# Performance work log

Hardware: AMD Instinct MI355X
Metric: run time of the kernel (lower is better)

## Reference

```python
import jax, jax.numpy as jnp
import numpy as np

N = 50000
E = 800000
D_IN = 384
D_H = 128
D_MLP = 128
K = 16


def layer_norm(x, g, b, eps=1e-5):
    m = x.mean(-1, keepdims=True)
    v = ((x - m) ** 2).mean(-1, keepdims=True)
    return (x - m) / jnp.sqrt(v + eps) * g + b


def setup_inputs() -> dict:
    key = jax.random.key(0)
    ks = jax.random.split(key, 16)
    s = lambda d: 1.0 / np.sqrt(d)
    return {
        "x": jax.random.normal(ks[0], (N, D_IN), jnp.float32),
        "edge_index": jax.random.randint(ks[1], (2, E), 0, N, jnp.int64),
        # GCNConv 1
        "W1": jax.random.normal(ks[2], (D_IN, D_H), jnp.float32) * s(D_IN),
        "b1": jnp.zeros((D_H,), jnp.float32),
        "g1": jnp.ones((D_H,), jnp.float32),
        "be1": jnp.zeros((D_H,), jnp.float32),
        # GCNConv 2
        "W2": jax.random.normal(ks[3], (D_H, D_H), jnp.float32) * s(D_H),
        "b2": jnp.zeros((D_H,), jnp.float32),
        "g2": jnp.ones((D_H,), jnp.float32),
        "be2": jnp.zeros((D_H,), jnp.float32),
        # residual projection (input_dim != conv_hidden)
        "rW": jax.random.normal(ks[4], (D_IN, D_H), jnp.float32) * s(D_IN),
        "rb": jnp.zeros((D_H,), jnp.float32),
        "rg": jnp.ones((D_H,), jnp.float32),
        "rbe": jnp.zeros((D_H,), jnp.float32),
        # MLP head
        "mW1": jax.random.normal(ks[5], (D_H, D_MLP), jnp.float32) * s(D_H),
        "mb1": jnp.zeros((D_MLP,), jnp.float32),
        "mg": jnp.ones((D_MLP,), jnp.float32),
        "mbe": jnp.zeros((D_MLP,), jnp.float32),
        "mW2": jax.random.normal(ks[6], (D_MLP, K), jnp.float32) * s(D_MLP),
        "mb2": jnp.zeros((K,), jnp.float32),
    }


def reference(x, edge_index, W1, b1, g1, be1, W2, b2, g2, be2,
              rW, rb, rg, rbe, mW1, mb1, mg, mbe, mW2, mb2):
    n = x.shape[0]
    loops = jnp.arange(n, dtype=edge_index.dtype)
    src = jnp.concatenate([edge_index[0], loops])  # [E+N]
    dst = jnp.concatenate([edge_index[1], loops])
    # symmetric GCN normalization with self-loops
    deg = jax.ops.segment_sum(jnp.ones_like(src, x.dtype), dst, num_segments=n)
    dinv = jnp.where(deg > 0, jax.lax.rsqrt(deg), 0.0)
    norm = dinv[src] * dinv[dst]  # [E+N]

    def gcn_conv(h, W, b):
        hw = h @ W  # [N, D_H]
        msg = hw[src] * norm[:, None]  # gather + scale, [E+N, D_H]
        return jax.ops.segment_sum(msg, dst, num_segments=n) + b

    # layer 1 with projected residual
    h = jax.nn.elu(layer_norm(gcn_conv(x, W1, b1), g1, be1))
    h = h + layer_norm(x @ rW + rb, rg, rbe)
    # layer 2 with identity residual
    h = jax.nn.elu(layer_norm(gcn_conv(h, W2, b2), g2, be2)) + h
    # MLP head (dropout inactive in eval) + softmax over clusters
    z = jax.nn.elu(layer_norm(h @ mW1 + mb1, mg, mbe))
    H = z @ mW2 + mb2
    return jax.nn.softmax(H, axis=1)
```

## Files before the change

kernel.cpp:

```cpp
#include <hip/hip_runtime.h>

#define DH 128

typedef __attribute__((ext_vector_type(8))) short short8;
typedef __attribute__((ext_vector_type(4))) float f32x4;

__device__ __forceinline__ float wave_sum(float v) {
    #pragma unroll
    for (int o = 32; o > 0; o >>= 1) v += __shfl_xor(v, o, 64);
    return v;
}

__device__ __forceinline__ void ln_pair(float v0, float v1, float& o0, float& o1) {
    float m = wave_sum(v0 + v1) * (1.f / 128.f);
    float d0 = v0 - m, d1 = v1 - m;
    float var = wave_sum(d0 * d0 + d1 * d1) * (1.f / 128.f);
    float inv = rsqrtf(var + 1e-5f);
    o0 = d0 * inv; o1 = d1 * inv;
}

__device__ __forceinline__ float elu(float x) { return x > 0.f ? x : expm1f(x); }

__device__ __forceinline__ unsigned short f2bf(float f) {
    unsigned u = __float_as_uint(f);
    u += 0x7fffu + ((u >> 16) & 1u);
    return (unsigned short)(u >> 16);
}
__device__ __forceinline__ float bfl(unsigned u) { return __uint_as_float(u << 16); }
__device__ __forceinline__ float bfh(unsigned u) { return __uint_as_float(u & 0xffff0000u); }
__device__ __forceinline__ unsigned pack_bf2(float a, float b) {
    return (unsigned)f2bf(a) | ((unsigned)f2bf(b) << 16);
}
__device__ __forceinline__ short8 cvt8(float4 v0, float4 v1) {
    short8 o;
    o[0] = (short)f2bf(v0.x); o[1] = (short)f2bf(v0.y);
    o[2] = (short)f2bf(v0.z); o[3] = (short)f2bf(v0.w);
    o[4] = (short)f2bf(v1.x); o[5] = (short)f2bf(v1.y);
    o[6] = (short)f2bf(v1.z); o[7] = (short)f2bf(v1.w);
    return o;
}

__device__ __forceinline__ int xcd_work(int bid, int nwg) {
    int qc = nwg >> 3, rc = nwg & 7;
    int xcd = bid & 7, ix = bid >> 3;
    return (xcd < rc ? xcd * (qc + 1) : rc * (qc + 1) + (xcd - rc) * qc) + ix;
}

__device__ __forceinline__ void gload_lds16(const void* gp, void* lp) {
    __builtin_amdgcn_global_load_lds(
        (const __attribute__((address_space(1))) void*)gp,
        (__attribute__((address_space(3))) void*)lp, 16, 0, 0);
}

__global__ void deg_count_k(const int* __restrict__ dst, int* __restrict__ deg, int E) {
    int e = blockIdx.x * 256 + threadIdx.x;
    if (e < E) atomicAdd(&deg[dst[e]], 1);
}

__global__ __launch_bounds__(1024) void scan_part_k(const int* __restrict__ deg,
                                                    int* __restrict__ rowptr,
                                                    int* __restrict__ bsum,
                                                    float* __restrict__ dinv, int n)
{
    __shared__ int wsum[16];
    const int tid = threadIdx.x, lane = tid & 63, wid = tid >> 6;
    int i = blockIdx.x * 1024 + tid;
    int v = (i < n) ? deg[i] : 0;
    if (i < n) dinv[i] = rsqrtf((float)(v + 1));
    int s = v;
    #pragma unroll
    for (int o = 1; o < 64; o <<= 1) {
        int t = __shfl_up(s, o, 64);
        if (lane >= o) s += t;
    }
    if (lane == 63) wsum[wid] = s;
    __syncthreads();
    if (tid < 16) {
        int ws = wsum[tid];
        #pragma unroll
        for (int o = 1; o < 16; o <<= 1) {
            int t = __shfl_up(ws, o, 64);
            if (tid >= o) ws += t;
        }
        wsum[tid] = ws;
    }
    __syncthreads();
    int excl = (wid ? wsum[wid - 1] : 0) + s - v;
    if (i < n) rowptr[i] = excl;
    if (tid == 0) bsum[blockIdx.x] = wsum[15];
}

__global__ void scan_top_k(int* __restrict__ bsum, int* __restrict__ rowptr_n, int nb) {
    int lane = threadIdx.x;
    int carry = 0;
    for (int base = 0; base < nb; base += 64) {
        int i = base + lane;
        int v = (i < nb) ? bsum[i] : 0;
        int s = v;
        #pragma unroll
        for (int o = 1; o < 64; o <<= 1) {
            int t = __shfl_up(s, o, 64);
            if (lane >= o) s += t;
        }
        if (i < nb) bsum[i] = carry + s - v;
        carry += __shfl(s, 63, 64);
    }
    if (lane == 0) *rowptr_n = carry;
}

__global__ void scan_add_k(const int* __restrict__ bsum, int* __restrict__ rowptr,
                           int* __restrict__ cursor, int n)
{
    int i = blockIdx.x * 256 + threadIdx.x;
    if (i < n) {
        int v = rowptr[i] + bsum[i >> 10];
        rowptr[i] = v;
        cursor[i] = v;
    }
}

__global__ __launch_bounds__(256) void fill_xcd_k(
    const int* __restrict__ src, const int* __restrict__ dst,
    const float* __restrict__ dinv, int* __restrict__ cursor,
    int2* __restrict__ csr, int E, int n)
{
    const int g   = blockIdx.x & 7;
    const int j   = blockIdx.x >> 3;
    const int bpg = gridDim.x >> 3;
    const int per = (n + 7) >> 3;
    const int lo = g * per;
    const int hi = min(n, lo + per);
    for (int e = j * 256 + threadIdx.x; e < E; e += bpg * 256) {
        int d = dst[e];
        if (d >= lo && d < hi) {
            int s = src[e];
            float w = dinv[s] * dinv[d];
            int p = atomicAdd(&cursor[d], 1);
            csr[p] = make_int2(s, __float_as_int(w));
        }
    }
}

__global__ void repack_zero_k(const float* __restrict__ W1, const float* __restrict__ rW,
                              const float* __restrict__ W2, const float* __restrict__ mW1,
                              unsigned short* __restrict__ Wp, int* __restrict__ deg, int n)
{
    int idx = blockIdx.x * 256 + threadIdx.x;
    if (idx < n) deg[idx] = 0;
    if (idx >= 131072) return;
    const float* W; int base;
    if (idx < 49152)       { W = W1;  base = 0; }
    else if (idx < 98304)  { W = rW;  base = 49152; }
    else if (idx < 114688) { W = W2;  base = 98304; }
    else                   { W = mW1; base = 114688; }
    int l = idx - base;
    int kb = l >> 12, rem = l & 4095;
    int nn = rem >> 5, ki = rem & 31;
    Wp[idx] = f2bf(W[(kb * 32 + ki) * DH + nn]);
}

__global__ __launch_bounds__(256, 2) void gemm1_k(
    const float* __restrict__ x,
    const unsigned short* __restrict__ Bp1, const unsigned short* __restrict__ Bp2,
    const float* __restrict__ bb,
    unsigned short* __restrict__ outa, unsigned short* __restrict__ outb, int n)
{
    constexpr int NT = 6;
    __shared__ __align__(16) unsigned char smraw[81920];
    float* smA = (float*)smraw;
    unsigned short* smB = (unsigned short*)(smraw + 65536);

    const int tid = threadIdx.x;
    const int wid = tid >> 6, lane = tid & 63;
    const int m16 = lane & 15, q = lane >> 4;

    const int work = xcd_work(blockIdx.x, gridDim.x);
    const int rblk = work >> 2;
    const int var  = work & 3;
    const int mat = var >> 1;
    const int c0  = (var & 1) * 64;
    const unsigned short* Bp = mat ? Bp2 : Bp1;
    unsigned short* outp = mat ? outb : outa;
    const float* bias = mat ? bb : nullptr;
    const long long rowbase = (long long)rblk * 128;

    const float* gA[8];
    int ldsA[8];
    #pragma unroll
    for (int i = 0; i < 8; ++i) {
        int j = wid * 8 + i;
        int r = j * 4 + (lane >> 4);
        int c = lane & 15;
        long long gr = rowbase + r; if (gr > (long long)n - 1) gr = n - 1;
        gA[i] = x + gr * 384 + ((c ^ (r & 15)) * 4);
        ldsA[i] = j * 256;
    }
    const unsigned short* gB[2];
    int ldsB[2];
    #pragma unroll
    for (int i = 0; i < 2; ++i) {
        int j2 = wid * 2 + i;
        int cl = j2 * 8 + (lane >> 3);
        int c = lane & 7;
        int cp = c ^ (cl & 7);
        gB[i] = Bp + (cp >> 2) * 4096 + (c0 + cl) * 32 + (cp & 3) * 8;
        ldsB[i] = j2 * 512;
    }

    auto issueT = [&](int t, int buf) {
        #pragma unroll
        for (int i = 0; i < 8; ++i)
            gload_lds16(gA[i] + t * 64, smA + buf * 8192 + ldsA[i]);
        #pragma unroll
        for (int i = 0; i < 2; ++i)
            gload_lds16(gB[i] + t * 8192, smB + buf * 4096 + ldsB[i]);
    };

    f32x4 acc[2][4];
    const f32x4 zero = {0.f, 0.f, 0.f, 0.f};
    #pragma unroll
    for (int mi = 0; mi < 2; ++mi)
        #pragma unroll
        for (int nj = 0; nj < 4; ++nj) acc[mi][nj] = zero;

    const int arow = wid * 32 + m16;
    const int s8b = m16 & 7;

    issueT(0, 0);
    __syncthreads();

    #pragma unroll
    for (int t = 0; t < NT; ++t) {
        const int buf = t & 1;
        if (t + 1 < NT) issueT(t + 1, buf ^ 1);
        const float* a0 = smA + buf * 8192;
        const unsigned short* b0 = smB + buf * 4096;
        short8 af[2][2], bf[2][4];
        #pragma unroll
        for (int ks = 0; ks < 2; ++ks) {
            int g0 = ks * 8 + q * 2;
            {
                float4 lo = *(const float4*)(a0 + arow * 64 + ((g0 ^ m16) * 4));
                float4 hi = *(const float4*)(a0 + arow * 64 + (((g0 + 1) ^ m16) * 4));
                af[ks][0] = cvt8(lo, hi);
            }
            {
                float4 lo = *(const float4*)(a0 + (arow + 16) * 64 + ((g0 ^ m16) * 4));
                float4 hi = *(const float4*)(a0 + (arow + 16) * 64 + (((g0 + 1) ^ m16) * 4));
                af[ks][1] = cvt8(lo, hi);
            }
            int co = ((ks * 4 + q) ^ s8b) * 8;
            #pragma unroll
            for (int nj = 0; nj < 4; ++nj)
                bf[ks][nj] = *(const short8*)(b0 + (nj * 16 + m16) * 64 + co);
        }
        #pragma unroll
        for (int ks = 0; ks < 2; ++ks)
            #pragma unroll
            for (int nj = 0; nj < 4; ++nj) {
                acc[0][nj] = __builtin_amdgcn_mfma_f32_16x16x32_bf16(af[ks][0], bf[ks][nj], acc[0][nj], 0, 0, 0);
                acc[1][nj] = __builtin_amdgcn_mfma_f32_16x16x32_bf16(af[ks][1], bf[ks][nj], acc[1][nj], 0, 0, 0);
            }
        __syncthreads();
    }

    unsigned short* ep = (unsigned short*)smraw;
    #pragma unroll
    for (int nj = 0; nj < 4; ++nj) {
        int cl = nj * 16 + m16;
        float bv = bias ? bias[c0 + cl] : 0.f;
        #pragma unroll
        for (int mi = 0; mi < 2; ++mi)
            #pragma unroll
            for (int r = 0; r < 4; ++r)
                ep[(wid * 32 + mi * 16 + q * 4 + r) * 72 + cl] = f2bf(acc[mi][nj][r] + bv);
    }
    __syncthreads();
    #pragma unroll
    for (int h = 0; h < 4; ++h) {
        int idx = tid + h * 256;
        int row = idx >> 3, c8 = idx & 7;
        long long grow = rowbase + row;
        if (grow < n)
            *(short8*)(outp + grow * DH + c0 + c8 * 8) = *(const short8*)(ep + row * 72 + c8 * 8);
    }
}

__global__ __launch_bounds__(256, 3) void gemm_k128(
    const unsigned short* __restrict__ A,
    const unsigned short* __restrict__ Bp, const float* __restrict__ bias,
    unsigned short* __restrict__ outp, int n)
{
    __shared__ __align__(16) unsigned short smem[24576];
    unsigned short* smB = smem + 16384;

    const int tid = threadIdx.x;
    const int wid = tid >> 6, lane = tid & 63;
    const int m16 = lane & 15, q = lane >> 4;

    const int work = xcd_work(blockIdx.x, gridDim.x);
    const int rblk = work >> 1;
    const int c0 = (work & 1) * 64;
    const long long rowbase = (long long)rblk * 128;

    #pragma unroll
    for (int r = 0; r < 8; ++r) {
        int j = r * 256 + tid;
        int row = j >> 4, c16 = j & 15;
        long long grow = rowbase + row; if (grow > (long long)n - 1) grow = n - 1;
        *(short8*)(smem + row * 128 + ((c16 ^ (row & 15)) * 8)) =
            *(const short8*)(A + grow * 128 + c16 * 8);
    }
    #pragma unroll
    for (int r = 0; r < 4; ++r) {
        int j = r * 256 + tid;
        int kb = j >> 8, rem = j & 255;
        int cl = rem >> 2, qq = rem & 3;
        *(short8*)(smB + kb * 2048 + qq * 512 + cl * 8) =
            *(const short8*)(Bp + kb * 4096 + c0 * 32 + rem * 8);
    }
    __syncthreads();

    f32x4 acc[2][4];
    const f32x4 zero = {0.f, 0.f, 0.f, 0.f};
    #pragma unroll
    for (int mi = 0; mi < 2; ++mi)
        #pragma unroll
        for (int nj = 0; nj < 4; ++nj) acc[mi][nj] = zero;

    const int frow = wid * 32 + m16;
    #pragma unroll
    for (int kb = 0; kb < 4; ++kb) {
        short8 af0 = *(const short8*)(smem + frow * 128 + (((kb * 4 + q) ^ m16) * 8));
        short8 af1 = *(const short8*)(smem + (frow + 16) * 128 + (((kb * 4 + q) ^ m16) * 8));
        #pragma unroll
        for (int nj = 0; nj < 4; ++nj) {
            short8 bf = *(const short8*)(smB + kb * 2048 + q * 512 + (nj * 16 + m16) * 8);
            acc[0][nj] = __builtin_amdgcn_mfma_f32_16x16x32_bf16(af0, bf, acc[0][nj], 0, 0, 0);
            acc[1][nj] = __builtin_amdgcn_mfma_f32_16x16x32_bf16(af1, bf, acc[1][nj], 0, 0, 0);
        }
    }

    __syncthreads();
    #pragma unroll
    for (int nj = 0; nj < 4; ++nj) {
        int cl = nj * 16 + m16;
        float bv = bias ? bias[c0 + cl] : 0.f;
        #pragma unroll
        for (int mi = 0; mi < 2; ++mi)
            #pragma unroll
            for (int r = 0; r < 4; ++r)
                smem[(wid * 32 + mi * 16 + q * 4 + r) * 72 + cl] = f2bf(acc[mi][nj][r] + bv);
    }
    __syncthreads();
    #pragma unroll
    for (int h = 0; h < 4; ++h) {
        int idx = tid + h * 256;
        int row = idx >> 3, c8 = idx & 7;
        long long grow = rowbase + row;
        if (grow < n)
            *(short8*)(outp + grow * DH + c0 + c8 * 8) = *(const short8*)(smem + row * 72 + c8 * 8);
    }
}

__device__ __forceinline__ void gather_row(
    const unsigned* __restrict__ hw, const int2* __restrict__ csr,
    int beg, int end, int lane, float& o0, float& o1)
{
    beg = __builtin_amdgcn_readfirstlane(beg);
    end = __builtin_amdgcn_readfirstlane(end);
    float a0 = 0.f, a1 = 0.f, b0 = 0.f, b1 = 0.f;
    float c0 = 0.f, c1 = 0.f, d0 = 0.f, d1 = 0.f;
    int p = beg;
    for (; p + 15 < end; p += 16) {
        int2 e[16];
        #pragma unroll
        for (int i = 0; i < 16; ++i) e[i] = csr[p + i];
        unsigned u[16];
        #pragma unroll
        for (int i = 0; i < 16; ++i) u[i] = hw[(long long)e[i].x * 64 + lane];
        #pragma unroll
        for (int i = 0; i < 16; ++i) {
            float w = __int_as_float(e[i].y);
            float lo = bfl(u[i]), hi = bfh(u[i]);
            if ((i & 3) == 0)      { a0 = fmaf(w, lo, a0); a1 = fmaf(w, hi, a1); }
            else if ((i & 3) == 1) { b0 = fmaf(w, lo, b0); b1 = fmaf(w, hi, b1); }
            else if ((i & 3) == 2) { c0 = fmaf(w, lo, c0); c1 = fmaf(w, hi, c1); }
            else                   { d0 = fmaf(w, lo, d0); d1 = fmaf(w, hi, d1); }
        }
    }
    for (; p + 3 < end; p += 4) {
        int2 e0 = csr[p], e1 = csr[p + 1], e2 = csr[p + 2], e3 = csr[p + 3];
        unsigned u0 = hw[(long long)e0.x * 64 + lane];
        unsigned u1 = hw[(long long)e1.x * 64 + lane];
        unsigned u2 = hw[(long long)e2.x * 64 + lane];
        unsigned u3 = hw[(long long)e3.x * 64 + lane];
        float w0 = __int_as_float(e0.y), w1 = __int_as_float(e1.y);
        float w2 = __int_as_float(e2.y), w3 = __int_as_float(e3.y);
        a0 = fmaf(w0, bfl(u0), a0);  a1 = fmaf(w0, bfh(u0), a1);
        b0 = fmaf(w1, bfl(u1), b0);  b1 = fmaf(w1, bfh(u1), b1);
        c0 = fmaf(w2, bfl(u2), c0);  c1 = fmaf(w2, bfh(u2), c1);
        d0 = fmaf(w3, bfl(u3), d0);  d1 = fmaf(w3, bfh(u3), d1);
    }
    for (; p < end; ++p) {
        int2 e0 = csr[p];
        unsigned u0 = hw[(long long)e0.x * 64 + lane];
        float w0 = __int_as_float(e0.y);
        a0 = fmaf(w0, bfl(u0), a0);
        a1 = fmaf(w0, bfh(u0), a1);
    }
    o0 = (a0 + b0) + (c0 + d0);
    o1 = (a1 + b1) + (c1 + d1);
}

__global__ __launch_bounds__(256) void gfuse1_k(
    const unsigned* __restrict__ hw, const unsigned* __restrict__ proj,
    const int* __restrict__ rowptr, const int2* __restrict__ csr,
    const float* __restrict__ dinv,
    const float* __restrict__ b1, const float* __restrict__ g1, const float* __restrict__ be1,
    const float* __restrict__ rg, const float* __restrict__ rbe,
    unsigned* __restrict__ hout, int n)
{
    int row = blockIdx.x * 4 + (threadIdx.x >> 6);
    if (row >= n) return;
    int lane = threadIdx.x & 63;
    float a0, a1;
    gather_row(hw, csr, rowptr[row], rowptr[row + 1], lane, a0, a1);
    long long off = (long long)row * 64;
    float di = dinv[row], sl = di * di;
    unsigned us = hw[off + lane];
    float2 bv  = *(const float2*)(b1 + 2 * lane);
    float2 gv  = *(const float2*)(g1 + 2 * lane);
    float2 bev = *(const float2*)(be1 + 2 * lane);
    float2 rgv = *(const float2*)(rg + 2 * lane);
    float2 rbv = *(const float2*)(rbe + 2 * lane);
    float v0 = a0 + sl * bfl(us) + bv.x;
    float v1 = a1 + sl * bfh(us) + bv.y;
    float o0, o1; ln_pair(v0, v1, o0, o1);
    float t0 = elu(o0 * gv.x + bev.x);
    float t1 = elu(o1 * gv.y + bev.y);
    unsigned up = proj[off + lane];
    float q0, q1; ln_pair(bfl(up), bfh(up), q0, q1);
    hout[off + lane] = pack_bf2(t0 + q0 * rgv.x + rbv.x, t1 + q1 * rgv.y + rbv.y);
}

__global__ __launch_bounds__(256) void gfuse2_k(
    const unsigned* __restrict__ hw, const unsigned* __restrict__ hprev,
    const int* __restrict__ rowptr, const int2* __restrict__ csr,
    const float* __restrict__ dinv,
    const float* __restrict__ b2, const float* __restrict__ g2, const float* __restrict__ be2,
    unsigned* __restrict__ h2, int n)
{
    int row = blockIdx.x * 4 + (threadIdx.x >> 6);
    if (row >= n) return;
    int lane = threadIdx.x & 63;
    float a0, a1;
    gather_row(hw, csr, rowptr[row], rowptr[row + 1], lane, a0, a1);
    long long off = (long long)row * 64;
    float di = dinv[row], sl = di * di;
    unsigned us = hw[off + lane];
    float2 bv  = *(const float2*)(b2 + 2 * lane);
    float2 gv  = *(const float2*)(g2 + 2 * lane);
    float2 bev = *(const float2*)(be2 + 2 * lane);
    float v0 = a0 + sl * bfl(us) + bv.x;
    float v1 = a1 + sl * bfh(us) + bv.y;
    float o0, o1; ln_pair(v0, v1, o0, o1);
    float t0 = elu(o0 * gv.x + bev.x);
    float t1 = elu(o1 * gv.y + bev.y);
    unsigned uh = hprev[off + lane];
    h2[off + lane] = pack_bf2(t0 + bfl(uh), t1 + bfh(uh));
}

__global__ __launch_bounds__(256) void head_k(
    const unsigned* __restrict__ zraw, const float* __restrict__ g, const float* __restrict__ be,
    const float* __restrict__ mW2, const float* __restrict__ mb2,
    float* __restrict__ out, int n)
{
    int row = blockIdx.x * 4 + (threadIdx.x >> 6);
    if (row >= n) return;
    int lane = threadIdx.x & 63;
    unsigned u = zraw[(long long)row * 64 + lane];
    float o0, o1; ln_pair(bfl(u), bfh(u), o0, o1);
    float2 gv  = *(const float2*)(g + 2 * lane);
    float2 bev = *(const float2*)(be + 2 * lane);
    float z0 = elu(o0 * gv.x + bev.x);
    float z1 = elu(o1 * gv.y + bev.y);
    int k = lane & 15, seg = lane >> 4;
    float acc = 0.f;
    #pragma unroll
    for (int t = 0; t < 16; ++t) {
        int srcl = seg * 16 + t;
        float zz0 = __shfl(z0, srcl, 64);
        float zz1 = __shfl(z1, srcl, 64);
        int c = seg * 32 + 2 * t;
        acc = fmaf(zz0, mW2[c * 16 + k], acc);
        acc = fmaf(zz1, mW2[(c + 1) * 16 + k], acc);
    }
    acc += __shfl_xor(acc, 32, 64);
    acc += __shfl_xor(acc, 16, 64);
    float hk = acc + mb2[k];
    float mx = hk;
    #pragma unroll
    for (int o = 8; o > 0; o >>= 1) mx = fmaxf(mx, __shfl_xor(mx, o, 64));
    float e = expf(hk - mx);
    float s = e;
    #pragma unroll
    for (int o = 8; o > 0; o >>= 1) s += __shfl_xor(s, o, 64);
    if (lane < 16) out[(long long)row * 16 + k] = e / s;
}

static inline size_t align16(size_t x) { return (x + 15) & ~(size_t)15; }

extern "C" void kernel_launch(void* const* d_in, const int* in_sizes, int n_in,
                              void* d_out, int out_size, void* d_ws, size_t ws_size,
                              hipStream_t stream)
{
    const float* x   = (const float*)d_in[0];
    const int*   ei  = (const int*)d_in[1];
    const float* W1  = (const float*)d_in[2];
    const float* b1  = (const float*)d_in[3];
    const float* g1  = (const float*)d_in[4];
    const float* be1 = (const float*)d_in[5];
    const float* W2  = (const float*)d_in[6];
    const float* b2  = (const float*)d_in[7];
    const float* g2  = (const float*)d_in[8];
    const float* be2 = (const float*)d_in[9];
    const float* rW  = (const float*)d_in[10];
    const float* rb  = (const float*)d_in[11];
    const float* rg  = (const float*)d_in[12];
    const float* rbe = (const float*)d_in[13];
    const float* mW1 = (const float*)d_in[14];
    const float* mb1 = (const float*)d_in[15];
    const float* mg  = (const float*)d_in[16];
    const float* mbe = (const float*)d_in[17];
    const float* mW2 = (const float*)d_in[18];
    const float* mb2 = (const float*)d_in[19];
    float* out = (float*)d_out;

    const int n = in_sizes[0] / 384;
    const int E = in_sizes[1] / 2;
    const int* src = ei;
    const int* dst = ei + E;

    char* w = (char*)d_ws;
    int* deg     = (int*)w;   w += align16((size_t)n * 4);
    int* rowptr  = (int*)w;   w += align16((size_t)(n + 1) * 4);
    int* cursor  = (int*)w;   w += align16((size_t)n * 4);
    float* dinv  = (float*)w; w += align16((size_t)n * 4);
    int* bsum    = (int*)w;   w += align16((size_t)1024 * 4);
    int2* csr    = (int2*)w;  w += align16((size_t)E * 8);
    unsigned short* hw1  = (unsigned short*)w; w += align16((size_t)n * DH * 2);
    unsigned short* proj = (unsigned short*)w; w += align16((size_t)n * DH * 2);
    unsigned short* hbuf = (unsigned short*)w; w += align16((size_t)n * DH * 2);
    unsigned short* Wp   = (unsigned short*)w; w += align16((size_t)131072 * 2);
    unsigned short* Wp1 = Wp;
    unsigned short* Wpr = Wp + 49152;
    unsigned short* Wp2 = Wp + 98304;
    unsigned short* WpM = Wp + 114688;
    unsigned short* hw2  = hw1;
    unsigned short* h2   = proj;
    unsigned short* zraw = hbuf;

    int gE = (E + 255) / 256;
    int gN = (n + 255) / 256;
    int nb = (n + 1023) / 1024;
    int rblks = (n + 127) / 128;
    int gRow4 = (n + 3) / 4;

    repack_zero_k<<<512, 256, 0, stream>>>(W1, rW, W2, mW1, Wp, deg, n);

    deg_count_k<<<gE, 256, 0, stream>>>(dst, deg, E);
    scan_part_k<<<nb, 1024, 0, stream>>>(deg, rowptr, bsum, dinv, n);
    scan_top_k<<<1, 64, 0, stream>>>(bsum, rowptr + n, nb);
    scan_add_k<<<gN, 256, 0, stream>>>(bsum, rowptr, cursor, n);
    fill_xcd_k<<<1024, 256, 0, stream>>>(src, dst, dinv, cursor, csr, E, n);

    gemm1_k<<<rblks * 4, 256, 0, stream>>>(x, Wp1, Wpr, rb, hw1, proj, n);
    gfuse1_k<<<gRow4, 256, 0, stream>>>((unsigned*)hw1, (unsigned*)proj, rowptr, csr, dinv,
                                        b1, g1, be1, rg, rbe, (unsigned*)hbuf, n);

    gemm_k128<<<rblks * 2, 256, 0, stream>>>(hbuf, Wp2, nullptr, hw2, n);
    gfuse2_k<<<gRow4, 256, 0, stream>>>((unsigned*)hw2, (unsigned*)hbuf, rowptr, csr, dinv,
                                        b2, g2, be2, (unsigned*)h2, n);

    gemm_k128<<<rblks * 2, 256, 0, stream>>>(h2, WpM, mb1, zraw, n);
    head_k<<<gRow4, 256, 0, stream>>>((unsigned*)zraw, mg, mbe, mW2, mb2, out, n);
}
```

Measured before the change: 408.1 us.

## Triple-buffer gemm1 with smaller K tiles and partition degree atomics by XCD

The first GEMM now uses 32-wide K tiles (12 steps) in a three-stage LDS ring with explicit vmcnt waits and raw barriers. Prefetch runs two tiles ahead, and the next load is issued after the fragment reads, so global loads overlap the MFMAs and one barrier per step is dropped. LDS use drops from 80KB to 60KB. The degree-count kernel becomes a grid-stride loop in which each XCD group counts only destinations in its own node range, keeping atomics local to one L2. In exchange, every group reads the whole dst array.

```diff
diff --git a/kernel.cpp b/kernel.cpp
--- a/kernel.cpp
+++ b/kernel.cpp
@@ -52,9 +52,19 @@
         (__attribute__((address_space(3))) void*)lp, 16, 0, 0);
 }
 
-__global__ void deg_count_k(const int* __restrict__ dst, int* __restrict__ deg, int E) {
-    int e = blockIdx.x * 256 + threadIdx.x;
-    if (e < E) atomicAdd(&deg[dst[e]], 1);
+__global__ __launch_bounds__(256) void deg_xcd_k(
+    const int* __restrict__ dst, int* __restrict__ deg, int E, int n)
+{
+    const int g   = blockIdx.x & 7;
+    const int j   = blockIdx.x >> 3;
+    const int bpg = gridDim.x >> 3;
+    const int per = (n + 7) >> 3;
+    const int lo = g * per;
+    const int hi = min(n, lo + per);
+    for (int e = j * 256 + threadIdx.x; e < E; e += bpg * 256) {
+        int d = dst[e];
+        if (d >= lo && d < hi) atomicAdd(&deg[d], 1);
+    }
 }
 
 __global__ __launch_bounds__(1024) void scan_part_k(const int* __restrict__ deg,
@@ -165,10 +175,8 @@
     const float* __restrict__ bb,
     unsigned short* __restrict__ outa, unsigned short* __restrict__ outb, int n)
 {
-    constexpr int NT = 6;
-    __shared__ __align__(16) unsigned char smraw[81920];
-    float* smA = (float*)smraw;
-    unsigned short* smB = (unsigned short*)(smraw + 65536);
+    constexpr int NT = 12;
+    __shared__ __align__(16) unsigned char smraw[61440];
 
     const int tid = threadIdx.x;
     const int wid = tid >> 6, lane = tid & 63;
@@ -177,43 +185,34 @@
     const int work = xcd_work(blockIdx.x, gridDim.x);
     const int rblk = work >> 2;
     const int var  = work & 3;
-    const int mat = var >> 1;
-    const int c0  = (var & 1) * 64;
+    const int mat  = var >> 1;
+    const int c0   = (var & 1) * 64;
     const unsigned short* Bp = mat ? Bp2 : Bp1;
     unsigned short* outp = mat ? outb : outa;
     const float* bias = mat ? bb : nullptr;
     const long long rowbase = (long long)rblk * 128;
 
-    const float* gA[8];
-    int ldsA[8];
-    #pragma unroll
-    for (int i = 0; i < 8; ++i) {
-        int j = wid * 8 + i;
-        int r = j * 4 + (lane >> 4);
-        int c = lane & 15;
+    const float* gA[4];
+    int abase[4];
+    #pragma unroll
+    for (int i = 0; i < 4; ++i) {
+        int j = wid * 4 + i;
+        int r = j * 8 + (lane >> 3);
+        int c = lane & 7;
         long long gr = rowbase + r; if (gr > (long long)n - 1) gr = n - 1;
-        gA[i] = x + gr * 384 + ((c ^ (r & 15)) * 4);
-        ldsA[i] = j * 256;
-    }
-    const unsigned short* gB[2];
-    int ldsB[2];
-    #pragma unroll
-    for (int i = 0; i < 2; ++i) {
-        int j2 = wid * 2 + i;
-        int cl = j2 * 8 + (lane >> 3);
-        int c = lane & 7;
-        int cp = c ^ (cl & 7);
-        gB[i] = Bp + (cp >> 2) * 4096 + (c0 + cl) * 32 + (cp & 3) * 8;
-        ldsB[i] = j2 * 512;
-    }
-
-    auto issueT = [&](int t, int buf) {
-        #pragma unroll
-        for (int i = 0; i < 8; ++i)
-            gload_lds16(gA[i] + t * 64, smA + buf * 8192 + ldsA[i]);
-        #pragma unroll
-        for (int i = 0; i < 2; ++i)
-            gload_lds16(gB[i] + t * 8192, smB + buf * 4096 + ldsB[i]);
+        gA[i] = x + gr * 384 + ((c ^ (r & 7)) * 4);
+        abase[i] = j * 1024;
+    }
+    const int clB = wid * 16 + (lane >> 2), cB = lane & 3;
+    const unsigned short* gB = Bp + (long long)(c0 + clB) * 32 + ((cB ^ (clB & 3)) * 8);
+    const int bbase = 16384 + wid * 1024;
+
+    auto issueT = [&](int t, int s) {
+        unsigned char* sb = smraw + s * 20480;
+        #pragma unroll
+        for (int i = 0; i < 4; ++i)
+            gload_lds16(gA[i] + t * 32, sb + abase[i]);
+        gload_lds16(gB + t * 4096, sb + bbase);
     };
 
     f32x4 acc[2][4];
@@ -224,46 +223,46 @@
         for (int nj = 0; nj < 4; ++nj) acc[mi][nj] = zero;
 
     const int arow = wid * 32 + m16;
-    const int s8b = m16 & 7;
 
     issueT(0, 0);
-    __syncthreads();
+    issueT(1, 1);
 
     #pragma unroll
     for (int t = 0; t < NT; ++t) {
-        const int buf = t & 1;
-        if (t + 1 < NT) issueT(t + 1, buf ^ 1);
-        const float* a0 = smA + buf * 8192;
-        const unsigned short* b0 = smB + buf * 4096;
-        short8 af[2][2], bf[2][4];
-        #pragma unroll
-        for (int ks = 0; ks < 2; ++ks) {
-            int g0 = ks * 8 + q * 2;
-            {
-                float4 lo = *(const float4*)(a0 + arow * 64 + ((g0 ^ m16) * 4));
-                float4 hi = *(const float4*)(a0 + arow * 64 + (((g0 + 1) ^ m16) * 4));
-                af[ks][0] = cvt8(lo, hi);
-            }
-            {
-                float4 lo = *(const float4*)(a0 + (arow + 16) * 64 + ((g0 ^ m16) * 4));
-                float4 hi = *(const float4*)(a0 + (arow + 16) * 64 + (((g0 + 1) ^ m16) * 4));
-                af[ks][1] = cvt8(lo, hi);
-            }
-            int co = ((ks * 4 + q) ^ s8b) * 8;
-            #pragma unroll
-            for (int nj = 0; nj < 4; ++nj)
-                bf[ks][nj] = *(const short8*)(b0 + (nj * 16 + m16) * 64 + co);
-        }
-        #pragma unroll
-        for (int ks = 0; ks < 2; ++ks)
-            #pragma unroll
-            for (int nj = 0; nj < 4; ++nj) {
-                acc[0][nj] = __builtin_amdgcn_mfma_f32_16x16x32_bf16(af[ks][0], bf[ks][nj], acc[0][nj], 0, 0, 0);
-                acc[1][nj] = __builtin_amdgcn_mfma_f32_16x16x32_bf16(af[ks][1], bf[ks][nj], acc[1][nj], 0, 0, 0);
-            }
-        __syncthreads();
-    }
-
+        const int s = t % 3;
+        if (t < NT - 1) asm volatile("s_waitcnt vmcnt(5)" ::: "memory");
+        else            asm volatile("s_waitcnt vmcnt(0)" ::: "memory");
+        __builtin_amdgcn_s_barrier();
+
+        const float* a0 = (const float*)(smraw + s * 20480);
+        const unsigned short* b0 = (const unsigned short*)(smraw + s * 20480 + 16384);
+        short8 af[2], bf[4];
+        #pragma unroll
+        for (int mi = 0; mi < 2; ++mi) {
+            int r = arow + mi * 16;
+            int s7 = r & 7;
+            float4 lo = *(const float4*)(a0 + r * 32 + (((2 * q) ^ s7) * 4));
+            float4 hi = *(const float4*)(a0 + r * 32 + (((2 * q + 1) ^ s7) * 4));
+            af[mi] = cvt8(lo, hi);
+        }
+        #pragma unroll
+        for (int nj = 0; nj < 4; ++nj) {
+            int cl = nj * 16 + m16;
+            bf[nj] = *(const short8*)(b0 + cl * 32 + ((q ^ (cl & 3)) * 8));
+        }
+        asm volatile("s_waitcnt lgkmcnt(0)" ::: "memory");
+        __builtin_amdgcn_sched_barrier(0);
+
+        if (t + 2 < NT) issueT(t + 2, (t + 2) % 3);
+
+        #pragma unroll
+        for (int nj = 0; nj < 4; ++nj) {
+            acc[0][nj] = __builtin_amdgcn_mfma_f32_16x16x32_bf16(af[0], bf[nj], acc[0][nj], 0, 0, 0);
+            acc[1][nj] = __builtin_amdgcn_mfma_f32_16x16x32_bf16(af[1], bf[nj], acc[1][nj], 0, 0, 0);
+        }
+    }
+
+    __syncthreads();
     unsigned short* ep = (unsigned short*)smraw;
     #pragma unroll
     for (int nj = 0; nj < 4; ++nj) {
@@ -561,7 +560,6 @@
     unsigned short* h2   = proj;
     unsigned short* zraw = hbuf;
 
-    int gE = (E + 255) / 256;
     int gN = (n + 255) / 256;
     int nb = (n + 1023) / 1024;
     int rblks = (n + 127) / 128;
@@ -569,7 +567,7 @@
 
     repack_zero_k<<<512, 256, 0, stream>>>(W1, rW, W2, mW1, Wp, deg, n);
 
-    deg_count_k<<<gE, 256, 0, stream>>>(dst, deg, E);
+    deg_xcd_k<<<1024, 256, 0, stream>>>(dst, deg, E, n);
     scan_part_k<<<nb, 1024, 0, stream>>>(deg, rowptr, bsum, dinv, n);
     scan_top_k<<<1, 64, 0, stream>>>(bsum, rowptr + n, nb);
     scan_add_k<<<gN, 256, 0, stream>>>(bsum, rowptr, cursor, n);
```

After: 408.6 us. No clear change (+0.1%).
